# Kernel tuning notes

Hardware: AMD Instinct MI355X
Metric: run time of the kernel (lower is better)

The kernel has to match this reference:

```python
import jax, jax.numpy as jnp
import numpy as np

SEQ = 2048          # prompt length (x.size(0) > 1 path)
D_IN = 4096         # weight.size(1)
N_OUT = 11008       # weight.size(0), Llama-7B FFN width
SPARSITY = 0.4      # fraction of neurons kept globally
TOKEN_SPARSITY = 0.2  # per-token top-k fraction (common.get_core_neurons)


def setup_inputs() -> dict:
    key = jax.random.key(0)
    kx, kw, kb = jax.random.split(key, 3)
    x = jax.random.normal(kx, (SEQ, D_IN), dtype=jnp.float16)
    weight = jax.random.normal(kw, (N_OUT, D_IN), dtype=jnp.float16) * jnp.float16(0.02)
    bias = jax.random.normal(kb, (N_OUT,), dtype=jnp.float16) * jnp.float16(0.02)
    return {"x": x, "weight": weight, "bias": bias}


def get_core_neurons(true_value, token_sparsity, sparsity, n_neurons):
    # Per-token top-k activations -> count how often each neuron appears ->
    # keep the globally most frequent `sparsity * n_neurons` neurons (sorted).
    k_tok = int(token_sparsity * n_neurons)
    remained = int(sparsity * n_neurons)
    _, tok_idx = jax.lax.top_k(true_value.astype(jnp.float32), k_tok)  # [SEQ, k_tok]
    counts = jnp.zeros((n_neurons,), dtype=jnp.int32).at[tok_idx.reshape(-1)].add(1)
    _, core_idx = jax.lax.top_k(counts, remained)
    return jnp.sort(core_idx)


def reference(x, weight, bias):
    # Prompt path: full GEMM in fp16, then core-neuron selection + weight gather.
    true_value = x @ weight.T + bias                      # [SEQ, N_OUT] fp16
    core_idx = get_core_neurons(true_value, TOKEN_SPARSITY, SPARSITY, weight.shape[0])
    filtered_W = weight[core_idx, :]                      # [remained, D_IN]
    filtered_bias = bias[core_idx]                        # [remained]
    return true_value, filtered_W, filtered_bias
```

## Files before the change

kernel.cpp:

```cpp
#include <hip/hip_runtime.h>

typedef __attribute__((ext_vector_type(8))) _Float16 half8;
typedef __attribute__((ext_vector_type(4))) float floatx4;
typedef unsigned short us_t;

#define SEQ   2048
#define DIN   4096
#define NOUT  11008
#define KTOK  2201
#define NCORE 4403
#define NCHUNK 43

__device__ __forceinline__ unsigned pk2(float a, float b) {
  auto h = __builtin_amdgcn_cvt_pkrtz(a, b);
  return __builtin_bit_cast(unsigned, h);
}
__device__ __forceinline__ unsigned fkey32(unsigned u) {
  return u ^ ((u >> 31) ? 0xFFFFFFFFu : 0x80000000u);
}
__device__ __forceinline__ void gl2lds16(const us_t* g, us_t* l) {
  __builtin_amdgcn_global_load_lds(
      (const __attribute__((address_space(1))) unsigned int*)(g),
      (__attribute__((address_space(3))) unsigned int*)(l), 16, 0, 0);
}

__global__ __launch_bounds__(256) void cvt_f16(const float* __restrict__ src,
                                               unsigned* __restrict__ dst, int n8) {
  int i = blockIdx.x * 256 + threadIdx.x;
  if (i >= n8) return;
  const float4* s = (const float4*)src + (size_t)i * 2;
  float4 a = s[0], b = s[1];
  uint4 o = {pk2(a.x, a.y), pk2(a.z, a.w), pk2(b.x, b.y), pk2(b.z, b.w)};
  ((uint4*)dst)[i] = o;
}

__global__ __launch_bounds__(256) void gemm_f16(const us_t* __restrict__ X16,
                                                const us_t* __restrict__ W16,
                                                const float* __restrict__ Bias,
                                                float* __restrict__ C) {
  __shared__ __attribute__((aligned(16))) us_t As[128 * 32];
  __shared__ __attribute__((aligned(16))) us_t Bs[128 * 32];
  const int t = threadIdx.x;
  const int m0 = blockIdx.y * 128, n0 = blockIdx.x * 128;
  const int l = t & 63, w = t >> 6;
  const int r = l & 15, q = l >> 4;
  const int wm = (w >> 1) * 64, wn = (w & 1) * 64;

  const us_t* Ag = X16 + (size_t)(m0 + (t >> 2)) * DIN + (t & 3) * 8;
  const us_t* Bg = W16 + (size_t)(n0 + (t >> 2)) * DIN + (t & 3) * 8;
  us_t* la = As + t * 8;
  us_t* lb = Bs + t * 8;

  floatx4 acc[4][4] = {};
  const us_t* pa = As + (wm + r) * 32 + q * 8;
  const us_t* pb = Bs + (wn + r) * 32 + q * 8;

  for (int kt = 0; kt < DIN; kt += 32) {
    gl2lds16(Ag + kt, la);
    gl2lds16(Ag + kt + 64 * DIN, la + 2048);
    gl2lds16(Bg + kt, lb);
    gl2lds16(Bg + kt + 64 * DIN, lb + 2048);
    __syncthreads();
    half8 af[4];
#pragma unroll
    for (int im = 0; im < 4; ++im)
      af[im] = *(const half8*)(pa + im * 16 * 32);
#pragma unroll
    for (int in = 0; in < 4; ++in) {
      half8 bfv = *(const half8*)(pb + in * 16 * 32);
#pragma unroll
      for (int im = 0; im < 4; ++im)
        acc[im][in] = __builtin_amdgcn_mfma_f32_16x16x32_f16(af[im], bfv, acc[im][in], 0, 0, 0);
    }
    __syncthreads();
  }
#pragma unroll
  for (int in = 0; in < 4; ++in) {
    const int col = n0 + wn + in * 16 + r;
    const float bv = Bias[col];
#pragma unroll
    for (int im = 0; im < 4; ++im) {
      const int row = m0 + wm + im * 16 + q * 4;
#pragma unroll
      for (int i = 0; i < 4; ++i)
        C[(size_t)(row + i) * NOUT + col] = acc[im][in][i] + bv;
    }
  }
}

__global__ __launch_bounds__(256) void gemm_bias(const float* __restrict__ X,
                                                 const float* __restrict__ W,
                                                 const float* __restrict__ Bias,
                                                 float* __restrict__ C) {
  __shared__ __attribute__((aligned(16))) us_t As[128 * 32];
  __shared__ __attribute__((aligned(16))) us_t Bs[128 * 32];
  const int t = threadIdx.x;
  const int m0 = blockIdx.y * 128, n0 = blockIdx.x * 128;
  const int l = t & 63, w = t >> 6;
  const int r = l & 15, q = l >> 4;
  const int wm = (w >> 1) * 64, wn = (w & 1) * 64;
  const float* Ag = X + (size_t)(m0 + (t >> 2)) * DIN + (t & 3) * 8;
  const float* Bg = W + (size_t)(n0 + (t >> 2)) * DIN + (t & 3) * 8;
  us_t* la = As + t * 8;
  us_t* lb = Bs + t * 8;
  floatx4 acc[4][4] = {};
  const us_t* pa = As + (wm + r) * 32 + q * 8;
  const us_t* pb = Bs + (wn + r) * 32 + q * 8;
  for (int kt = 0; kt < DIN; kt += 32) {
    float4 a0 = *(const float4*)(Ag + kt);
    float4 a1 = *(const float4*)(Ag + kt + 4);
    float4 a2 = *(const float4*)(Ag + kt + 64 * DIN);
    float4 a3 = *(const float4*)(Ag + kt + 64 * DIN + 4);
    float4 b0 = *(const float4*)(Bg + kt);
    float4 b1 = *(const float4*)(Bg + kt + 4);
    float4 b2 = *(const float4*)(Bg + kt + 64 * DIN);
    float4 b3 = *(const float4*)(Bg + kt + 64 * DIN + 4);
    uint4 ua  = {pk2(a0.x, a0.y), pk2(a0.z, a0.w), pk2(a1.x, a1.y), pk2(a1.z, a1.w)};
    uint4 ua2 = {pk2(a2.x, a2.y), pk2(a2.z, a2.w), pk2(a3.x, a3.y), pk2(a3.z, a3.w)};
    uint4 ub  = {pk2(b0.x, b0.y), pk2(b0.z, b0.w), pk2(b1.x, b1.y), pk2(b1.z, b1.w)};
    uint4 ub2 = {pk2(b2.x, b2.y), pk2(b2.z, b2.w), pk2(b3.x, b3.y), pk2(b3.z, b3.w)};
    *(uint4*)la = ua;
    *(uint4*)(la + 2048) = ua2;
    *(uint4*)lb = ub;
    *(uint4*)(lb + 2048) = ub2;
    __syncthreads();
    half8 af[4];
#pragma unroll
    for (int im = 0; im < 4; ++im)
      af[im] = *(const half8*)(pa + im * 16 * 32);
#pragma unroll
    for (int in = 0; in < 4; ++in) {
      half8 bfv = *(const half8*)(pb + in * 16 * 32);
#pragma unroll
      for (int im = 0; im < 4; ++im)
        acc[im][in] = __builtin_amdgcn_mfma_f32_16x16x32_f16(af[im], bfv, acc[im][in], 0, 0, 0);
    }
    __syncthreads();
  }
#pragma unroll
  for (int in = 0; in < 4; ++in) {
    const int col = n0 + wn + in * 16 + r;
    const float bv = Bias[col];
#pragma unroll
    for (int im = 0; im < 4; ++im) {
      const int row = m0 + wm + im * 16 + q * 4;
#pragma unroll
      for (int i = 0; i < 4; ++i)
        C[(size_t)(row + i) * NOUT + col] = acc[im][in][i] + bv;
    }
  }
}

__global__ __launch_bounds__(256) void row_topk(const float* __restrict__ TV,
                                                int* __restrict__ counts) {
  __shared__ __attribute__((aligned(16))) unsigned keys[NOUT];
  __shared__ int hist[2048];
  __shared__ int csum[256];
  __shared__ int shv[2];
  __shared__ int cnte[NCHUNK * 4];
  const int t = threadIdx.x;
  const int lane = t & 63, wv = t >> 6;

  for (int i = t; i < 2048; i += 256) hist[i] = 0;
  __syncthreads();
  const uint4* src = (const uint4*)(TV + (size_t)blockIdx.x * NOUT);
  for (int i = t; i < NOUT / 4; i += 256) {
    uint4 v = src[i];
    unsigned k0 = fkey32(v.x), k1 = fkey32(v.y), k2 = fkey32(v.z), k3 = fkey32(v.w);
    uint4 kk = {k0, k1, k2, k3};
    *(uint4*)&keys[i * 4] = kk;
    atomicAdd(&hist[k0 >> 21], 1);
    atomicAdd(&hist[k1 >> 21], 1);
    atomicAdd(&hist[k2 >> 21], 1);
    atomicAdd(&hist[k3 >> 21], 1);
  }
  __syncthreads();
  { int s = 0; for (int j = 0; j < 8; ++j) s += hist[t * 8 + j]; csum[t] = s; }
  __syncthreads();
  if (t == 0) {
    int cum = 0;
    for (int c = 255; c >= 0; --c) {
      if (cum + csum[c] >= KTOK) {
        for (int v = c * 8 + 7; v >= c * 8; --v) {
          if (cum + hist[v] >= KTOK) { shv[0] = v; shv[1] = cum; break; }
          cum += hist[v];
        }
        break;
      }
      cum += csum[c];
    }
  }
  __syncthreads();
  const unsigned b1 = (unsigned)shv[0];
  const int above1 = shv[1];
  __syncthreads();

  for (int i = t; i < 2048; i += 256) hist[i] = 0;
  __syncthreads();
  for (int i = t; i < NOUT; i += 256) {
    unsigned k = keys[i];
    if ((k >> 21) == b1) atomicAdd(&hist[(k >> 10) & 0x7FF], 1);
  }
  __syncthreads();
  { int s = 0; for (int j = 0; j < 8; ++j) s += hist[t * 8 + j]; csum[t] = s; }
  __syncthreads();
  if (t == 0) {
    int cum = above1;
    for (int c = 255; c >= 0; --c) {
      if (cum + csum[c] >= KTOK) {
        for (int v = c * 8 + 7; v >= c * 8; --v) {
          if (cum + hist[v] >= KTOK) { shv[0] = v; shv[1] = cum; break; }
          cum += hist[v];
        }
        break;
      }
      cum += csum[c];
    }
  }
  __syncthreads();
  const unsigned b2 = (unsigned)shv[0];
  const int above2 = shv[1];
  const unsigned pref2 = (b1 << 11) | b2;
  __syncthreads();

  for (int i = t; i < 1024; i += 256) hist[i] = 0;
  __syncthreads();
  for (int i = t; i < NOUT; i += 256) {
    unsigned k = keys[i];
    if ((k >> 10) == pref2) atomicAdd(&hist[k & 0x3FF], 1);
  }
  __syncthreads();
  { int s = 0; if (t < 128) { for (int j = 0; j < 8; ++j) s += hist[t * 8 + j]; } csum[t] = s; }
  __syncthreads();
  if (t == 0) {
    int cum = above2;
    for (int c = 127; c >= 0; --c) {
      if (cum + csum[c] >= KTOK) {
        for (int v = c * 8 + 7; v >= c * 8; --v) {
          if (cum + hist[v] >= KTOK) { shv[0] = v; shv[1] = cum; break; }
          cum += hist[v];
        }
        break;
      }
      cum += csum[c];
    }
  }
  __syncthreads();
  const unsigned T = (pref2 << 10) | (unsigned)shv[0];
  const int need = KTOK - shv[1];

  for (int c = 0; c < NCHUNK; ++c) {
    const int i = c * 256 + t;
    const unsigned k = keys[i];
    if (k > T) atomicAdd(&counts[i], 1);
    unsigned long long me = __ballot(k == T);
    if (lane == 0) cnte[c * 4 + wv] = __popcll(me);
  }
  __syncthreads();
  for (int c = 0; c < NCHUNK; ++c) {
    const int i = c * 256 + t;
    const unsigned k = keys[i];
    const bool eq = (k == T);
    unsigned long long me = __ballot(eq);
    if (eq) {
      int rank = __popcll(me & ((1ULL << lane) - 1));
      const int idx = c * 4 + wv;
      for (int j = 0; j < idx; ++j) rank += cnte[j];
      if (rank < need) atomicAdd(&counts[i], 1);
    }
  }
}

__global__ __launch_bounds__(256) void select_core(const int* __restrict__ counts,
                                                   const float* __restrict__ Bias,
                                                   int* __restrict__ core_idx,
                                                   float* __restrict__ bias_out) {
  __shared__ int cl[NOUT];
  __shared__ int hist[2049];
  __shared__ int csum[257];
  __shared__ int shv[2];
  __shared__ int tabS[256];
  const int t = threadIdx.x;
  const int lane = t & 63, wv = t >> 6;
  for (int i = t; i < NOUT; i += 256) cl[i] = counts[i];
  for (int i = t; i < 2049; i += 256) hist[i] = 0;
  tabS[t] = 0;
  __syncthreads();
  for (int i = t; i < NOUT; i += 256) atomicAdd(&hist[cl[i]], 1);
  __syncthreads();
  { int s = 0; for (int j = 0; j < 8; ++j) s += hist[t * 8 + j]; csum[t] = s;
    if (t == 0) csum[256] = hist[2048]; }
  __syncthreads();
  if (t == 0) {
    int cum = 0;
    for (int c = 256; c >= 0; --c) {
      if (cum + csum[c] >= NCORE) {
        int hi = (c == 256) ? 2048 : c * 8 + 7;
        for (int v = hi; v >= c * 8; --v) {
          if (cum + hist[v] >= NCORE) { shv[0] = v; shv[1] = NCORE - cum; break; }
          cum += hist[v];
        }
        break;
      }
      cum += csum[c];
    }
  }
  __syncthreads();
  const int Cv = shv[0], need2 = shv[1];
  for (int c = 0; c < NCHUNK; ++c) {
    const int i = c * 256 + t;
    const int cnt = cl[i];
    unsigned long long mg = __ballot(cnt > Cv);
    unsigned long long me = __ballot(cnt == Cv);
    if (lane == 0) tabS[c * 4 + wv] = __popcll(mg) | (__popcll(me) << 16);
  }
  __syncthreads();
  int orig = tabS[t];
  for (int off = 1; off < 256; off <<= 1) {
    int v = (t >= off) ? tabS[t - off] : 0;
    __syncthreads();
    tabS[t] += v;
    __syncthreads();
  }
  int excl = tabS[t] - orig;
  __syncthreads();
  tabS[t] = excl;
  __syncthreads();
  const unsigned long long lm = (1ULL << lane) - 1;
  for (int c = 0; c < NCHUNK; ++c) {
    const int i = c * 256 + t;
    const int cnt = cl[i];
    const bool g = cnt > Cv, e = cnt == Cv;
    unsigned long long mg = __ballot(g);
    unsigned long long me = __ballot(e);
    const int P = tabS[c * 4 + wv];
    const int gpre = (P & 0xFFFF) + __popcll(mg & lm);
    const int epre = (P >> 16) + __popcll(me & lm);
    const bool sel = g || (e && epre < need2);
    if (sel) {
      const int pos = gpre + (epre < need2 ? epre : need2);
      core_idx[pos] = i;
      bias_out[pos] = Bias[i];
    }
  }
}

__global__ __launch_bounds__(256) void gather_rows(const float* __restrict__ W,
                                                   const int* __restrict__ core_idx,
                                                   float* __restrict__ outW) {
  const int b = blockIdx.x;
  const int j = core_idx[b];
  const float4* src = (const float4*)(W + (size_t)j * DIN);
  float4* dst = (float4*)(outW + (size_t)b * DIN);
  for (int i = threadIdx.x; i < DIN / 4; i += 256) dst[i] = src[i];
}

__global__ __launch_bounds__(256) void zero_counts(int* __restrict__ counts) {
  counts[blockIdx.x * 256 + threadIdx.x] = 0;
}

extern "C" void kernel_launch(void* const* d_in, const int* in_sizes, int n_in,
                              void* d_out, int out_size, void* d_ws, size_t ws_size,
                              hipStream_t stream) {
  const float* X    = (const float*)d_in[0];
  const float* W    = (const float*)d_in[1];
  const float* Bias = (const float*)d_in[2];
  float* out_tv = (float*)d_out;
  float* out_w  = out_tv + (size_t)SEQ * NOUT;
  float* out_b  = out_w + (size_t)NCORE * DIN;
  int* counts   = (int*)d_ws;
  int* core_idx = counts + NOUT;

  const size_t meta = 64 * 1024;
  const size_t need_ws = meta + ((size_t)SEQ * DIN + (size_t)NOUT * DIN) * sizeof(us_t);

  zero_counts<<<NOUT / 256, 256, 0, stream>>>(counts);
  if (ws_size >= need_ws) {
    us_t* X16 = (us_t*)((char*)d_ws + meta);
    us_t* W16 = X16 + (size_t)SEQ * DIN;
    cvt_f16<<<(SEQ * DIN / 8 + 255) / 256, 256, 0, stream>>>(X, (unsigned*)X16, SEQ * DIN / 8);
    cvt_f16<<<(NOUT * DIN / 8 + 255) / 256, 256, 0, stream>>>(W, (unsigned*)W16, NOUT * DIN / 8);
    gemm_f16<<<dim3(NOUT / 128, SEQ / 128), 256, 0, stream>>>(X16, W16, Bias, out_tv);
  } else {
    gemm_bias<<<dim3(NOUT / 128, SEQ / 128), 256, 0, stream>>>(X, W, Bias, out_tv);
  }
  row_topk<<<SEQ, 256, 0, stream>>>(out_tv, counts);
  select_core<<<1, 256, 0, stream>>>(counts, Bias, core_idx, out_b);
  gather_rows<<<NCORE, 256, 0, stream>>>(W, core_idx, out_w);
}
```

Measured before the change: 804.6 us.

## Double-buffer LDS tiles in fp16 GEMM and remap blocks across XCDs

```diff
diff --git a/kernel.cpp b/kernel.cpp
--- a/kernel.cpp
+++ b/kernel.cpp
@@ -10,6 +10,7 @@
 #define KTOK  2201
 #define NCORE 4403
 #define NCHUNK 43
+#define NBLK  1376
 
 __device__ __forceinline__ unsigned pk2(float a, float b) {
   auto h = __builtin_amdgcn_cvt_pkrtz(a, b);
@@ -38,42 +39,86 @@
                                                 const us_t* __restrict__ W16,
                                                 const float* __restrict__ Bias,
                                                 float* __restrict__ C) {
-  __shared__ __attribute__((aligned(16))) us_t As[128 * 32];
-  __shared__ __attribute__((aligned(16))) us_t Bs[128 * 32];
+  __shared__ __attribute__((aligned(16))) us_t As[2][128 * 32];
+  __shared__ __attribute__((aligned(16))) us_t Bs[2][128 * 32];
   const int t = threadIdx.x;
-  const int m0 = blockIdx.y * 128, n0 = blockIdx.x * 128;
+
+  const int id = blockIdx.x;
+  const int wg = ((id & 7) * (NBLK / 8)) + (id >> 3);
+  const int m0 = (wg / 86) * 128;
+  const int n0 = (wg % 86) * 128;
+
   const int l = t & 63, w = t >> 6;
   const int r = l & 15, q = l >> 4;
   const int wm = (w >> 1) * 64, wn = (w & 1) * 64;
 
   const us_t* Ag = X16 + (size_t)(m0 + (t >> 2)) * DIN + (t & 3) * 8;
   const us_t* Bg = W16 + (size_t)(n0 + (t >> 2)) * DIN + (t & 3) * 8;
-  us_t* la = As + t * 8;
-  us_t* lb = Bs + t * 8;
+  us_t* la0 = &As[0][t * 8];
+  us_t* la1 = &As[1][t * 8];
+  us_t* lb0 = &Bs[0][t * 8];
+  us_t* lb1 = &Bs[1][t * 8];
 
   floatx4 acc[4][4] = {};
-  const us_t* pa = As + (wm + r) * 32 + q * 8;
-  const us_t* pb = Bs + (wn + r) * 32 + q * 8;
-
-  for (int kt = 0; kt < DIN; kt += 32) {
-    gl2lds16(Ag + kt, la);
-    gl2lds16(Ag + kt + 64 * DIN, la + 2048);
-    gl2lds16(Bg + kt, lb);
-    gl2lds16(Bg + kt + 64 * DIN, lb + 2048);
-    __syncthreads();
+  const us_t* pa0 = &As[0][(wm + r) * 32 + q * 8];
+  const us_t* pa1 = &As[1][(wm + r) * 32 + q * 8];
+  const us_t* pb0 = &Bs[0][(wm + r) * 32 + q * 8];
+  const us_t* pb0n = &Bs[0][(wn + r) * 32 + q * 8];
+  const us_t* pb1n = &Bs[1][(wn + r) * 32 + q * 8];
+  (void)pb0;
+
+  auto stage = [&](us_t* la_, us_t* lb_, int kt) {
+    gl2lds16(Ag + kt, la_);
+    gl2lds16(Ag + kt + 64 * DIN, la_ + 2048);
+    gl2lds16(Bg + kt, lb_);
+    gl2lds16(Bg + kt + 64 * DIN, lb_ + 2048);
+  };
+  auto compute = [&](const us_t* pa_, const us_t* pb_) {
     half8 af[4];
 #pragma unroll
     for (int im = 0; im < 4; ++im)
-      af[im] = *(const half8*)(pa + im * 16 * 32);
+      af[im] = *(const half8*)(pa_ + im * 16 * 32);
 #pragma unroll
     for (int in = 0; in < 4; ++in) {
-      half8 bfv = *(const half8*)(pb + in * 16 * 32);
+      half8 bfv = *(const half8*)(pb_ + in * 16 * 32);
 #pragma unroll
       for (int im = 0; im < 4; ++im)
         acc[im][in] = __builtin_amdgcn_mfma_f32_16x16x32_f16(af[im], bfv, acc[im][in], 0, 0, 0);
     }
-    __syncthreads();
-  }
+  };
+
+  stage(la0, lb0, 0);
+  stage(la1, lb1, 32);
+
+  for (int kt = 0; kt < DIN - 64; kt += 64) {
+    asm volatile("s_waitcnt vmcnt(4)" ::: "memory");
+    __builtin_amdgcn_s_barrier();
+    __builtin_amdgcn_sched_barrier(0);
+    compute(pa0, pb0n);
+    __builtin_amdgcn_sched_barrier(0);
+    __builtin_amdgcn_s_barrier();
+    __builtin_amdgcn_sched_barrier(0);
+    stage(la0, lb0, kt + 64);
+
+    asm volatile("s_waitcnt vmcnt(4)" ::: "memory");
+    __builtin_amdgcn_s_barrier();
+    __builtin_amdgcn_sched_barrier(0);
+    compute(pa1, pb1n);
+    __builtin_amdgcn_sched_barrier(0);
+    __builtin_amdgcn_s_barrier();
+    __builtin_amdgcn_sched_barrier(0);
+    stage(la1, lb1, kt + 96);
+  }
+  asm volatile("s_waitcnt vmcnt(4)" ::: "memory");
+  __builtin_amdgcn_s_barrier();
+  __builtin_amdgcn_sched_barrier(0);
+  compute(pa0, pb0n);
+  __builtin_amdgcn_sched_barrier(0);
+  asm volatile("s_waitcnt vmcnt(0)" ::: "memory");
+  __builtin_amdgcn_s_barrier();
+  __builtin_amdgcn_sched_barrier(0);
+  compute(pa1, pb1n);
+
 #pragma unroll
   for (int in = 0; in < 4; ++in) {
     const int col = n0 + wn + in * 16 + r;
@@ -380,7 +425,7 @@
     us_t* W16 = X16 + (size_t)SEQ * DIN;
     cvt_f16<<<(SEQ * DIN / 8 + 255) / 256, 256, 0, stream>>>(X, (unsigned*)X16, SEQ * DIN / 8);
     cvt_f16<<<(NOUT * DIN / 8 + 255) / 256, 256, 0, stream>>>(W, (unsigned*)W16, NOUT * DIN / 8);
-    gemm_f16<<<dim3(NOUT / 128, SEQ / 128), 256, 0, stream>>>(X16, W16, Bias, out_tv);
+    gemm_f16<<<NBLK, 256, 0, stream>>>(X16, W16, Bias, out_tv);
   } else {
     gemm_bias<<<dim3(NOUT / 128, SEQ / 128), 256, 0, stream>>>(X, W, Bias, out_tv);
   }
```

Measured after the change: 852.7 us. 6.0% more time.
